# Performance work log

Hardware: AMD Instinct MI355X
Metric: run time of the kernel (lower is better)

The kernel has to match this reference:

```python
import jax, jax.numpy as jnp
import numpy as np


def _rotate_every_two(x):
    # interleaved pairs: (x0, x1) -> (-x1, x0)
    x1 = x[..., ::2]
    x2 = x[..., 1::2]
    return jnp.stack((-x2, x1), axis=-1).reshape(x.shape)


def setup_inputs() -> dict:
    key = jax.random.key(0)
    ks = jax.random.split(key, 6)
    B, S, D = 2, 2048, 1024
    w = lambda k, shape: jax.random.normal(k, shape, dtype=jnp.float32) * 0.02
    return {
        "x": jax.random.normal(ks[0], (B, S, D), dtype=jnp.float32),
        "Wq": w(ks[1], (D, D)), "bq": jnp.zeros((D,), jnp.float32),
        "Wk": w(ks[2], (D, D)), "bk": jnp.zeros((D,), jnp.float32),
        "Wv": w(ks[3], (D, 2 * D)), "bv": jnp.zeros((2 * D,), jnp.float32),
        "Wg": w(ks[4], (D, 2 * D)), "bg": jnp.zeros((2 * D,), jnp.float32),
        "Wo": w(ks[5], (2 * D, D)), "bo": jnp.zeros((D,), jnp.float32),
    }


def reference(x, Wq, bq, Wk, bk, Wv, bv, Wg, bg, Wo, bo):
    B, S, D = x.shape
    H = 16
    key_dim = D // H          # 64
    head_dim = 2 * D // H     # 128 (factor=2)
    scaling = key_dim ** -0.5

    # RetNetRelPos buffers (deterministic)
    angle = 1.0 / 10000.0 ** jnp.linspace(0.0, 1.0, key_dim // 2)
    angle = jnp.repeat(angle, 2).astype(jnp.float32)          # [key_dim]
    decay = jnp.log(1.0 - 2.0 ** (-5.0 - jnp.arange(H, dtype=jnp.float32)))  # [H]

    idx = jnp.arange(S, dtype=jnp.float32)
    sin = jnp.sin(idx[:, None] * angle[None, :])              # [S, key_dim]
    cos = jnp.cos(idx[:, None] * angle[None, :])

    # causal exponential decay mask, normalized by sqrt(rowsum)
    diff = idx[:, None] - idx[None, :]                        # [S, S]
    mask = jnp.where(diff >= 0, jnp.exp(decay[:, None, None] * diff), 0.0)  # [H,S,S]
    mask = mask / jnp.sqrt(mask.sum(-1, keepdims=True))

    q = (x @ Wq + bq).reshape(B, S, H, key_dim).transpose(0, 2, 1, 3)              # [B,H,S,kd]
    k = ((x @ Wk + bk) * scaling).reshape(B, S, H, key_dim).transpose(0, 2, 1, 3)
    v = x @ Wv + bv                                                                # [B,S,2D]
    g = x @ Wg + bg

    qr = q * cos + _rotate_every_two(q) * sin
    kr = k * cos + _rotate_every_two(k) * sin
    vr = v.reshape(B, S, H, head_dim).transpose(0, 2, 1, 3)                        # [B,H,S,hd]

    qk = jnp.einsum('bhsd,bhtd->bhst', qr, kr) * mask                              # [B,H,S,S]
    denom = jnp.clip(jnp.abs(jax.lax.stop_gradient(qk).sum(-1, keepdims=True)), 1.0, None)
    qk = qk / denom

    out = jnp.einsum('bhst,bhtd->bhsd', qk, vr).transpose(0, 2, 1, 3)              # [B,S,H,hd]

    # LayerNorm over head_dim, eps=1e-5, no affine (biased variance as in torch)
    mu = out.mean(-1, keepdims=True)
    var = ((out - mu) ** 2).mean(-1, keepdims=True)
    out = (out - mu) / jnp.sqrt(var + 1e-5)

    out = out.reshape(B, S, H * head_dim)                                          # [B,S,2D]
    out = jax.nn.silu(g) * out
    return out @ Wo + bo
```

## Files before the change

kernel.cpp:

```cpp
#include <hip/hip_runtime.h>
#include <hip/hip_bf16.h>

typedef __attribute__((ext_vector_type(8))) unsigned short ushort8;
typedef __attribute__((ext_vector_type(4))) float f32x4;
typedef __attribute__((ext_vector_type(8))) __bf16 bf16x8;
typedef unsigned int u32_g __attribute__((address_space(1)));
typedef unsigned int u32_l __attribute__((address_space(3)));

__device__ __forceinline__ float bf2f(unsigned short u) {
  union { unsigned u; float f; } v; v.u = ((unsigned)u) << 16; return v.f;
}
__device__ __forceinline__ unsigned short f2bf(float f) {
  union { float f; unsigned u; } v; v.f = f;
  unsigned r = v.u + 0x7FFFu + ((v.u >> 16) & 1u);
  return (unsigned short)(r >> 16);
}
__device__ __forceinline__ unsigned cvtpk_bf16(float lo, float hi) {
  unsigned r;
  asm("v_cvt_pk_bf16_f32 %0, %1, %2" : "=v"(r) : "v"(lo), "v"(hi));
  return r;
}
__device__ __forceinline__ f32x4 mfma16(bf16x8 a, bf16x8 b, f32x4 c) {
  return __builtin_amdgcn_mfma_f32_16x16x32_bf16(a, b, c, 0, 0, 0);
}
__device__ __forceinline__ void gload16(const void* g, void* l) {
  __builtin_amdgcn_global_load_lds((const u32_g*)g, (u32_l*)l, 16, 0, 0);
}

__global__ __launch_bounds__(256) void transpose_cast(
    const float* __restrict__ W, unsigned short* __restrict__ WT,
    int K, int N, int ldwt, int row_off)
{
  __shared__ unsigned short t[64 * 80];
  int n0 = blockIdx.x * 64, k0 = blockIdx.y * 64;
  int tid = threadIdx.x;
#pragma unroll
  for (int i = 0; i < 4; i++) {
    int c = tid + 256 * i;
    int r = c >> 4, q = c & 15;
    float4 v = *(const float4*)&W[(size_t)(k0 + r) * N + n0 + q * 4];
    t[(q * 4 + 0) * 80 + r] = f2bf(v.x);
    t[(q * 4 + 1) * 80 + r] = f2bf(v.y);
    t[(q * 4 + 2) * 80 + r] = f2bf(v.z);
    t[(q * 4 + 3) * 80 + r] = f2bf(v.w);
  }
  __syncthreads();
#pragma unroll
  for (int i = 0; i < 2; i++) {
    int c = tid + 256 * i;
    int n = c >> 3, p = c & 7;
    *(ushort8*)&WT[(size_t)(row_off + n0 + n) * ldwt + k0 + p * 8] =
        *(const ushort8*)&t[n * 80 + p * 8];
  }
}

__global__ void biascat_kernel(const float* __restrict__ bq, const float* __restrict__ bk,
                               const float* __restrict__ bv, const float* __restrict__ bg,
                               float* __restrict__ bcat)
{
  int i = blockIdx.x * 256 + threadIdx.x;
  float v;
  if (i < 1024) v = bq[i];
  else if (i < 2048) v = bk[i - 1024];
  else if (i < 4096) v = bv[i - 2048];
  else v = bg[i - 4096];
  bcat[i] = v;
}

__global__ void cast_x_kernel(const float* __restrict__ x, unsigned short* __restrict__ xb)
{
  size_t i = (size_t)(blockIdx.x * 256 + threadIdx.x) * 4;
  float4 v = *(const float4*)&x[i];
  unsigned r0 = (unsigned)f2bf(v.x) | ((unsigned)f2bf(v.y) << 16);
  unsigned r1 = (unsigned)f2bf(v.z) | ((unsigned)f2bf(v.w) << 16);
  uint2 o; o.x = r0; o.y = r1;
  *(uint2*)&xb[i] = o;
}

template<int OUT_BF16, int BN, int SM, int SN>
__global__ __launch_bounds__(256, 3) void gemm3_kernel(
    const unsigned short* __restrict__ A, const unsigned short* __restrict__ BT,
    const float* __restrict__ bias, void* __restrict__ Cout,
    int M, int N, int K)
{
  constexpr int BUFS = (128 + BN) * 32;
  constexpr int ACH  = 512;
  constexpr int LPS  = (128 + BN) / 64;
  constexpr int STB  = SM * SN;
  __shared__ __attribute__((aligned(16))) unsigned short lds[3 * BUFS];
  int tid = threadIdx.x, wave = tid >> 6, lane = tid & 63;
  int lr = lane & 15, lg = lane >> 4;
  int gx = gridDim.x;
  int lin = blockIdx.x + gx * blockIdx.y;
  int cpx = (gx * gridDim.y) >> 3;
  int xcd = lin & 7, s = lin >> 3;
  int spx = cpx / STB;
  int sup = xcd * spx + s / STB;
  int nSupN = gx / SN;
  int stm = sup / nSupN, stn = sup % nSupN;
  int idx = s % STB;
  int m0 = (stm * SM + idx / SN) * 128;
  int n0 = (stn * SN + idx % SN) * BN;
  int wr = (wave >> 1) * 64, wc = (wave & 1) * (BN / 2);
  constexpr int NR = BN / 32;

  const unsigned short* gsrc[LPS];
#pragma unroll
  for (int i = 0; i < LPS; i++) {
    int c = tid + i * 256;
    if (c < ACH) {
      int r = c >> 2, j = c & 3;
      gsrc[i] = A + (size_t)(m0 + r) * K + ((j ^ ((r >> 1) & 3)) << 3);
    } else {
      int c2 = c - ACH, r = c2 >> 2, j = c2 & 3;
      gsrc[i] = BT + (size_t)(n0 + r) * K + ((j ^ ((r >> 1) & 3)) << 3);
    }
  }

  auto stage = [&](int buf, int kt) {
    char* lb = (char*)(lds + buf * BUFS);
#pragma unroll
    for (int i = 0; i < LPS; i++)
      gload16(gsrc[i] + kt * 32, lb + (tid + i * 256) * 16);
  };

  f32x4 acc[4][NR] = {};
  int nk = K >> 5;
  stage(0, 0);
  stage(1, 1);
  int cb = 0;
  for (int it = 0; it < nk; it++) {
    if (it + 1 < nk) {
      if constexpr (LPS == 4) asm volatile("s_waitcnt vmcnt(4)" ::: "memory");
      else                    asm volatile("s_waitcnt vmcnt(3)" ::: "memory");
    } else {
      asm volatile("s_waitcnt vmcnt(0)" ::: "memory");
    }
    __builtin_amdgcn_sched_barrier(0);
    __builtin_amdgcn_s_barrier();
    __builtin_amdgcn_sched_barrier(0);
    if (it + 2 < nk) {
      int sb = cb + 2; if (sb >= 3) sb -= 3;
      stage(sb, it + 2);
    }
    const unsigned short* as = lds + cb * BUFS;
    const unsigned short* bs = as + 128 * 32;
    int csw = (lg ^ ((lr >> 1) & 3)) << 3;
    bf16x8 af[4], bfr[NR];
#pragma unroll
    for (int m = 0; m < 4; m++)
      af[m] = *(const bf16x8*)&as[(wr + m * 16 + lr) * 32 + csw];
#pragma unroll
    for (int n = 0; n < NR; n++)
      bfr[n] = *(const bf16x8*)&bs[(wc + n * 16 + lr) * 32 + csw];
    __builtin_amdgcn_s_setprio(1);
#pragma unroll
    for (int m = 0; m < 4; m++)
#pragma unroll
      for (int n = 0; n < NR; n++)
        acc[m][n] = mfma16(af[m], bfr[n], acc[m][n]);
    __builtin_amdgcn_s_setprio(0);
    cb++; if (cb == 3) cb = 0;
  }

#pragma unroll
  for (int m = 0; m < 4; m++) {
#pragma unroll
    for (int n = 0; n < NR; n++) {
      int col = n0 + wc + n * 16 + lr;
      float bv = bias ? bias[col] : 0.f;
#pragma unroll
      for (int r = 0; r < 4; r++) {
        int row = m0 + wr + m * 16 + lg * 4 + r;
        float v = acc[m][n][r] + bv;
        if (OUT_BF16)
          ((unsigned short*)Cout)[(size_t)row * N + col] = f2bf(v);
        else
          ((float*)Cout)[(size_t)row * N + col] = v;
      }
    }
  }
}

__global__ __launch_bounds__(256) void prep_qk_kernel(
    const unsigned short* __restrict__ Y,
    unsigned short* __restrict__ qr, unsigned short* __restrict__ kr)
{
  int t = blockIdx.x * 256 + threadIdx.x;
  int j = t & 31;
  int h = (t >> 5) & 15;
  int bs = t >> 9;
  int s = bs & 2047;
  int b = bs >> 11;
  float ang = __expf(-0.29710774f * (float)j);
  float th = (float)s * ang;
  float sn, cs;
  __sincosf(th, &sn, &cs);
  const unsigned short* yq = &Y[(size_t)bs * 6144 + h * 64 + 2 * j];
  unsigned qv = *(const unsigned*)yq;
  unsigned kv = *(const unsigned*)(yq + 1024);
  float q0 = bf2f((unsigned short)(qv & 0xffff));
  float q1 = bf2f((unsigned short)(qv >> 16));
  float k0 = bf2f((unsigned short)(kv & 0xffff)) * 0.125f;
  float k1 = bf2f((unsigned short)(kv >> 16)) * 0.125f;
  float qr0 = q0 * cs - q1 * sn, qr1 = q1 * cs + q0 * sn;
  float kr0 = k0 * cs - k1 * sn, kr1 = k1 * cs + k0 * sn;
  size_t o = ((size_t)(b * 16 + h) * 2048 + s) * 64 + 2 * j;
  *(unsigned*)&qr[o] = (unsigned)f2bf(qr0) | ((unsigned)f2bf(qr1) << 16);
  *(unsigned*)&kr[o] = (unsigned)f2bf(kr0) | ((unsigned)f2bf(kr1) << 16);
}

__global__ __launch_bounds__(256) void prep_v_kernel(
    const unsigned short* __restrict__ Y, unsigned short* __restrict__ vT)
{
  __shared__ unsigned short t[128 * 80];
  int s0 = blockIdx.x * 64;
  int bh = blockIdx.y;
  int b = bh >> 4, h = bh & 15;
  int tid = threadIdx.x;
#pragma unroll
  for (int i = 0; i < 4; i++) {
    int c = tid + 256 * i;
    int r = c >> 4, p = c & 15;
    ushort8 v = *(const ushort8*)&Y[(size_t)(b * 2048 + s0 + r) * 6144 + 2048 + h * 128 + p * 8];
#pragma unroll
    for (int e = 0; e < 8; e++) t[(p * 8 + e) * 80 + r] = v[e];
  }
  __syncthreads();
#pragma unroll
  for (int i = 0; i < 4; i++) {
    int c = tid + 256 * i;
    int d = c >> 3, p = c & 7;
    *(ushort8*)&vT[((size_t)bh * 128 + d) * 2048 + s0 + p * 8] = *(const ushort8*)&t[d * 80 + p * 8];
  }
}

#define LPAD 72
__global__ __launch_bounds__(256, 2) void retention_kernel(
    const unsigned short* __restrict__ qr, const unsigned short* __restrict__ kr,
    const unsigned short* __restrict__ vT, const unsigned short* __restrict__ Yg,
    unsigned short* __restrict__ Z)
{
  __shared__ __attribute__((aligned(16))) unsigned short lds[24576 + 4 * 16 * LPAD];
  unsigned short* const lk0 = lds;
  unsigned short* const lk1 = lds + 4096;
  unsigned short* const lv0 = lds + 8192;
  unsigned short* const lv1 = lds + 16384;
  unsigned short* const lp  = lds + 24576;

  int lin = blockIdx.x;
  int xcd = lin & 7, slot = lin >> 3;
  int bh = xcd + 8 * (slot >> 4);
  int bx = slot & 15;
  int b = bh >> 4, h = bh & 15;
  float decay = __logf(1.f - exp2f(-5.f - (float)h));
  int tid = threadIdx.x, wave = tid >> 6, lane = tid & 63;
  int lr = lane & 15, lg = lane >> 4;
  const unsigned short* qbase = &qr[(size_t)bh * 2048 * 64];
  const unsigned short* kbase = &kr[(size_t)bh * 2048 * 64];
  const unsigned short* vbase = &vT[(size_t)bh * 128 * 2048];
  unsigned short* lpw = &lp[wave * 16 * LPAD];
  int swz = (lr & 7) << 3;

  float cf[4][4];
#pragma unroll
  for (int nb = 0; nb < 4; nb++)
#pragma unroll
    for (int r = 0; r < 4; r++)
      cf[nb][r] = __expf(-decay * (float)(nb * 16 + lg * 4 + r));

  auto stage = [&](int bufi, int t0) {
    const char* kg = (const char*)(kbase + (size_t)t0 * 64);
    const char* vg = (const char*)vbase + (size_t)t0 * 2;
    char* lk = (char*)(bufi ? lk1 : lk0);
    char* lv = (char*)(bufi ? lv1 : lv0);
#pragma unroll
    for (int i = 0; i < 2; i++) {
      int c = tid + i * 256;
      int r = c >> 3, j = c & 7;
      gload16(kg + r * 128 + ((j ^ (r & 7)) << 4), lk + c * 16);
    }
#pragma unroll
    for (int i = 0; i < 4; i++) {
      int c = tid + i * 256;
      int d = c >> 3, j = c & 7;
      gload16(vg + (size_t)d * 4096 + ((j ^ (d & 7)) << 4), lv + c * 16);
    }
  };

  for (int pass = 0; pass < 2; pass++) {
    int stile = pass ? 31 - bx : bx;
    int s0 = stile * 64;
    int sq = s0 + wave * 16 + lr;
    bf16x8 qf0 = *(const bf16x8*)&qbase[(size_t)sq * 64 + lg * 8];
    bf16x8 qf1 = *(const bf16x8*)&qbase[(size_t)sq * 64 + 32 + lg * 8];
    f32x4 accv[8] = {};
    float rs = 0.f;
    int nt = stile + 1;

    stage(0, 0);
    __syncthreads();
    for (int it = 0; it < nt; it++) {
      int t0 = it * 64;
      if (it + 1 < nt) stage((it + 1) & 1, t0 + 64);
      const unsigned short* lk = (it & 1) ? lk1 : lk0;
      const unsigned short* lv = (it & 1) ? lv1 : lv0;
      bool bnd = (it == nt - 1);
      float rowf = __expf(decay * (float)(sq - t0));
#pragma unroll
      for (int nb = 0; nb < 4; nb++) {
        f32x4 sa = {};
        bf16x8 a0 = *(const bf16x8*)&lk[((nb * 16 + lr) * 64 + lg * 8) ^ swz];
        bf16x8 a1 = *(const bf16x8*)&lk[((nb * 16 + lr) * 64 + 32 + lg * 8) ^ swz];
        sa = mfma16(a0, qf0, sa);
        sa = mfma16(a1, qf1, sa);
        float pv[4];
#pragma unroll
        for (int r = 0; r < 4; r++) {
          float w = rowf * cf[nb][r];
          if (bnd) {
            int tt = t0 + nb * 16 + lg * 4 + r;
            w = (tt <= sq) ? w : 0.f;
          }
          pv[r] = sa[r] * w;
          rs += pv[r];
        }
        uint2 wv;
        wv.x = cvtpk_bf16(pv[0], pv[1]);
        wv.y = cvtpk_bf16(pv[2], pv[3]);
        *(uint2*)&lpw[lr * LPAD + nb * 16 + lg * 4] = wv;
      }
#pragma unroll
      for (int kk = 0; kk < 2; kk++) {
        bf16x8 pa = *(const bf16x8*)&lpw[lr * LPAD + kk * 32 + lg * 8];
#pragma unroll
        for (int nb = 0; nb < 8; nb++) {
          bf16x8 bv = *(const bf16x8*)&lv[((nb * 16 + lr) * 64 + kk * 32 + lg * 8) ^ swz];
          accv[nb] = mfma16(pa, bv, accv[nb]);
        }
      }
      __syncthreads();
    }

    rs += __shfl_xor(rs, 16);
    rs += __shfl_xor(rs, 32);
    int srb = s0 + wave * 16 + lg * 4;
    const unsigned short* gb2 = &Yg[((size_t)(b * 2048 + srb)) * 6144 + 4096 + h * 128];
    unsigned short* zb = &Z[((size_t)(b * 2048 + srb)) * 2048 + h * 128];
#pragma unroll
    for (int r = 0; r < 4; r++) {
      float rsq = __shfl(rs, lg * 4 + r);
      float sidx = (float)(srb + r);
      float geo = (1.f - __expf(decay * (sidx + 1.f))) * exp2f(5.f + (float)h);
      float invs = rsqrtf(geo);
      float den = fmaxf(fabsf(rsq * invs), 1.f);
      float scl = invs / den;
      float sm = 0.f, sq2 = 0.f;
#pragma unroll
      for (int nb = 0; nb < 8; nb++) {
        float v = accv[nb][r] * scl;
        sm += v; sq2 += v * v;
      }
      sm += __shfl_xor(sm, 1); sm += __shfl_xor(sm, 2);
      sm += __shfl_xor(sm, 4); sm += __shfl_xor(sm, 8);
      sq2 += __shfl_xor(sq2, 1); sq2 += __shfl_xor(sq2, 2);
      sq2 += __shfl_xor(sq2, 4); sq2 += __shfl_xor(sq2, 8);
      float mu = sm * (1.f / 128.f);
      float var = sq2 * (1.f / 128.f) - mu * mu;
      float istd = rsqrtf(var + 1e-5f);
#pragma unroll
      for (int nb = 0; nb < 8; nb++) {
        float v = accv[nb][r] * scl;
        float nrm = (v - mu) * istd;
        float g = bf2f(gb2[(size_t)r * 6144 + nb * 16 + lr]);
        float sg = g / (1.f + __expf(-g));
        zb[(size_t)r * 2048 + nb * 16 + lr] = f2bf(nrm * sg);
      }
    }
  }
}

extern "C" void kernel_launch(void* const* d_in, const int* in_sizes, int n_in,
                              void* d_out, int out_size, void* d_ws, size_t ws_size,
                              hipStream_t stream) {
  const float* x  = (const float*)d_in[0];
  const float* Wq = (const float*)d_in[1];
  const float* bq = (const float*)d_in[2];
  const float* Wk = (const float*)d_in[3];
  const float* bk = (const float*)d_in[4];
  const float* Wv = (const float*)d_in[5];
  const float* bv = (const float*)d_in[6];
  const float* Wg = (const float*)d_in[7];
  const float* bg = (const float*)d_in[8];
  const float* Wo = (const float*)d_in[9];
  const float* bo = (const float*)d_in[10];

  char* ws = (char*)d_ws;
  unsigned short* xbf   = (unsigned short*)(ws);
  unsigned short* wcatT = (unsigned short*)(ws + 8388608);
  unsigned short* woT   = (unsigned short*)(ws + 20971520);
  unsigned short* Y     = (unsigned short*)(ws + 25165824);
  unsigned short* qrb   = (unsigned short*)(ws + 75497472);
  unsigned short* krb   = (unsigned short*)(ws + 83886080);
  unsigned short* vT    = (unsigned short*)(ws + 92274688);
  float*          bcat  = (float*)(ws + 109051904);
  unsigned short* Z     = xbf;

  transpose_cast<<<dim3(16, 16), 256, 0, stream>>>(Wq, wcatT, 1024, 1024, 1024, 0);
  transpose_cast<<<dim3(16, 16), 256, 0, stream>>>(Wk, wcatT, 1024, 1024, 1024, 1024);
  transpose_cast<<<dim3(32, 16), 256, 0, stream>>>(Wv, wcatT, 1024, 2048, 1024, 2048);
  transpose_cast<<<dim3(32, 16), 256, 0, stream>>>(Wg, wcatT, 1024, 2048, 1024, 4096);
  transpose_cast<<<dim3(16, 32), 256, 0, stream>>>(Wo, woT, 2048, 1024, 2048, 0);
  biascat_kernel<<<24, 256, 0, stream>>>(bq, bk, bv, bg, bcat);
  cast_x_kernel<<<4096, 256, 0, stream>>>(x, xbf);

  gemm3_kernel<1, 128, 8, 6><<<dim3(48, 32), 256, 0, stream>>>(xbf, wcatT, bcat, Y, 4096, 6144, 1024);

  prep_qk_kernel<<<8192, 256, 0, stream>>>(Y, qrb, krb);
  prep_v_kernel<<<dim3(32, 32), 256, 0, stream>>>(Y, vT);

  retention_kernel<<<512, 256, 0, stream>>>(qrb, krb, vT, Y, Z);

  gemm3_kernel<0, 64, 4, 4><<<dim3(16, 32), 256, 0, stream>>>(Z, woT, bo, d_out, 4096, 1024, 2048);
}
```

Before: 197.1 us.

## Switch retention kernel to 32x32 MFMA with 128-row query tiles

Rewrites the retention kernel to use 32x32x16 bf16 MFMA instructions, with each wave owning 32 query rows and each block owning a 128-row query tile instead of two 64-row passes. Load balancing changes from pairing tiles within one head to pairing mirrored tiles across two heads. The P tile gets an XOR-swizzled LDS layout in place of padding. The aim is fewer LDS reads and MFMA issues per FLOP, since K/V tiles are reused across more query rows. The cost is more accumulator registers (4 f32x16) and a boundary mask that now covers two tiles.

```diff
diff --git a/kernel.cpp b/kernel.cpp
--- a/kernel.cpp
+++ b/kernel.cpp
@@ -3,6 +3,7 @@
 
 typedef __attribute__((ext_vector_type(8))) unsigned short ushort8;
 typedef __attribute__((ext_vector_type(4))) float f32x4;
+typedef __attribute__((ext_vector_type(16))) float f32x16;
 typedef __attribute__((ext_vector_type(8))) __bf16 bf16x8;
 typedef unsigned int u32_g __attribute__((address_space(1)));
 typedef unsigned int u32_l __attribute__((address_space(3)));
@@ -22,6 +23,9 @@
 }
 __device__ __forceinline__ f32x4 mfma16(bf16x8 a, bf16x8 b, f32x4 c) {
   return __builtin_amdgcn_mfma_f32_16x16x32_bf16(a, b, c, 0, 0, 0);
+}
+__device__ __forceinline__ f32x16 mfma32(bf16x8 a, bf16x8 b, f32x16 c) {
+  return __builtin_amdgcn_mfma_f32_32x32x16_bf16(a, b, c, 0, 0, 0);
 }
 __device__ __forceinline__ void gload16(const void* g, void* l) {
   __builtin_amdgcn_global_load_lds((const u32_g*)g, (u32_l*)l, 16, 0, 0);
@@ -235,13 +239,12 @@
   }
 }
 
-#define LPAD 72
 __global__ __launch_bounds__(256, 2) void retention_kernel(
     const unsigned short* __restrict__ qr, const unsigned short* __restrict__ kr,
     const unsigned short* __restrict__ vT, const unsigned short* __restrict__ Yg,
     unsigned short* __restrict__ Z)
 {
-  __shared__ __attribute__((aligned(16))) unsigned short lds[24576 + 4 * 16 * LPAD];
+  __shared__ __attribute__((aligned(16))) unsigned short lds[24576 + 4 * 32 * 64];
   unsigned short* const lk0 = lds;
   unsigned short* const lk1 = lds + 4096;
   unsigned short* const lv0 = lds + 8192;
@@ -249,25 +252,33 @@
   unsigned short* const lp  = lds + 24576;
 
   int lin = blockIdx.x;
-  int xcd = lin & 7, slot = lin >> 3;
-  int bh = xcd + 8 * (slot >> 4);
-  int bx = slot & 15;
+  int xcd = lin & 7, s = lin >> 3;
+  int par = s & 1, j = (s >> 1) & 15, bg = s >> 5;
+  int f  = par ? 15 - j : j;
+  int bh = xcd + 8 * (2 * bg + par);
   int b = bh >> 4, h = bh & 15;
   float decay = __logf(1.f - exp2f(-5.f - (float)h));
   int tid = threadIdx.x, wave = tid >> 6, lane = tid & 63;
-  int lr = lane & 15, lg = lane >> 4;
+  int lq = lane & 31, hi = lane >> 5;
   const unsigned short* qbase = &qr[(size_t)bh * 2048 * 64];
   const unsigned short* kbase = &kr[(size_t)bh * 2048 * 64];
   const unsigned short* vbase = &vT[(size_t)bh * 128 * 2048];
-  unsigned short* lpw = &lp[wave * 16 * LPAD];
-  int swz = (lr & 7) << 3;
-
-  float cf[4][4];
-#pragma unroll
-  for (int nb = 0; nb < 4; nb++)
-#pragma unroll
-    for (int r = 0; r < 4; r++)
-      cf[nb][r] = __expf(-decay * (float)(nb * 16 + lg * 4 + r));
+  unsigned short* lpw = &lp[wave * 32 * 64];
+  int kswz = lq & 7;
+  int pswz = (lq & 7) << 1;
+
+  int q0 = f * 128;
+  int sq = q0 + wave * 32 + lq;
+  bf16x8 qf[4];
+#pragma unroll
+  for (int ks = 0; ks < 4; ks++)
+    qf[ks] = *(const bf16x8*)&qbase[(size_t)sq * 64 + hi * 8 + ks * 16];
+
+  float cfA[16];
+#pragma unroll
+  for (int r = 0; r < 16; r++)
+    cfA[r] = __expf(-decay * (float)((r & 3) + 8 * (r >> 2) + 4 * hi));
+  float w32 = __expf(-decay * 32.f);
 
   auto stage = [&](int bufi, int t0) {
     const char* kg = (const char*)(kbase + (size_t)t0 * 64);
@@ -277,105 +288,114 @@
 #pragma unroll
     for (int i = 0; i < 2; i++) {
       int c = tid + i * 256;
-      int r = c >> 3, j = c & 7;
-      gload16(kg + r * 128 + ((j ^ (r & 7)) << 4), lk + c * 16);
+      int r = c >> 3, jj = c & 7;
+      gload16(kg + r * 128 + ((jj ^ (r & 7)) << 4), lk + c * 16);
     }
 #pragma unroll
     for (int i = 0; i < 4; i++) {
       int c = tid + i * 256;
-      int d = c >> 3, j = c & 7;
-      gload16(vg + (size_t)d * 4096 + ((j ^ (d & 7)) << 4), lv + c * 16);
+      int d = c >> 3, jj = c & 7;
+      gload16(vg + (size_t)d * 4096 + ((jj ^ (d & 7)) << 4), lv + c * 16);
     }
   };
 
-  for (int pass = 0; pass < 2; pass++) {
-    int stile = pass ? 31 - bx : bx;
-    int s0 = stile * 64;
-    int sq = s0 + wave * 16 + lr;
-    bf16x8 qf0 = *(const bf16x8*)&qbase[(size_t)sq * 64 + lg * 8];
-    bf16x8 qf1 = *(const bf16x8*)&qbase[(size_t)sq * 64 + 32 + lg * 8];
-    f32x4 accv[8] = {};
-    float rs = 0.f;
-    int nt = stile + 1;
-
-    stage(0, 0);
+  f32x16 accv[4] = {};
+  float rs = 0.f;
+  int nt = 2 * f + 2;
+
+  stage(0, 0);
+  __syncthreads();
+  for (int it = 0; it < nt; it++) {
+    int t0 = it * 64;
+    if (it + 1 < nt) stage((it + 1) & 1, t0 + 64);
+    const unsigned short* lk = (it & 1) ? lk1 : lk0;
+    const unsigned short* lv = (it & 1) ? lv1 : lv0;
+    bool bnd = (it >= nt - 2);
+    float rowf = __expf(decay * (float)(sq - t0));
+    f32x16 st0 = {}, st1 = {};
+#pragma unroll
+    for (int ks = 0; ks < 4; ks++) {
+      bf16x8 a0 = *(const bf16x8*)&lk[lq * 64 + (((hi + 2 * ks) ^ kswz) << 3)];
+      bf16x8 a1 = *(const bf16x8*)&lk[(32 + lq) * 64 + (((hi + 2 * ks) ^ kswz) << 3)];
+      st0 = mfma32(a0, qf[ks], st0);
+      st1 = mfma32(a1, qf[ks], st1);
+    }
+#pragma unroll
+    for (int tb = 0; tb < 2; tb++) {
+      float rf = tb ? rowf * w32 : rowf;
+#pragma unroll
+      for (int g = 0; g < 4; g++) {
+        float p0, p1, p2, p3;
+        {
+          float w0 = rf * cfA[g * 4 + 0];
+          float w1 = rf * cfA[g * 4 + 1];
+          float w2 = rf * cfA[g * 4 + 2];
+          float w3 = rf * cfA[g * 4 + 3];
+          if (bnd) {
+            int tb0 = t0 + 32 * tb + 8 * g + 4 * hi;
+            w0 = (tb0 + 0 <= sq) ? w0 : 0.f;
+            w1 = (tb0 + 1 <= sq) ? w1 : 0.f;
+            w2 = (tb0 + 2 <= sq) ? w2 : 0.f;
+            w3 = (tb0 + 3 <= sq) ? w3 : 0.f;
+          }
+          const f32x16& stv = tb ? st1 : st0;
+          p0 = stv[g * 4 + 0] * w0;
+          p1 = stv[g * 4 + 1] * w1;
+          p2 = stv[g * 4 + 2] * w2;
+          p3 = stv[g * 4 + 3] * w3;
+        }
+        rs += p0 + p1 + p2 + p3;
+        uint2 wv;
+        wv.x = cvtpk_bf16(p0, p1);
+        wv.y = cvtpk_bf16(p2, p3);
+        int c4 = (2 * g + hi + 8 * tb) ^ pswz;
+        *(uint2*)&lpw[lq * 64 + (c4 << 2)] = wv;
+      }
+    }
+#pragma unroll
+    for (int ts = 0; ts < 4; ts++) {
+      bf16x8 pa = *(const bf16x8*)&lpw[lq * 64 + ((((2 * hi + 4 * ts)) ^ pswz) << 2)];
+#pragma unroll
+      for (int nb = 0; nb < 4; nb++) {
+        bf16x8 vf = *(const bf16x8*)&lv[(nb * 32 + lq) * 64 + (((hi + 2 * ts) ^ kswz) << 3)];
+        accv[nb] = mfma32(pa, vf, accv[nb]);
+      }
+    }
     __syncthreads();
-    for (int it = 0; it < nt; it++) {
-      int t0 = it * 64;
-      if (it + 1 < nt) stage((it + 1) & 1, t0 + 64);
-      const unsigned short* lk = (it & 1) ? lk1 : lk0;
-      const unsigned short* lv = (it & 1) ? lv1 : lv0;
-      bool bnd = (it == nt - 1);
-      float rowf = __expf(decay * (float)(sq - t0));
-#pragma unroll
-      for (int nb = 0; nb < 4; nb++) {
-        f32x4 sa = {};
-        bf16x8 a0 = *(const bf16x8*)&lk[((nb * 16 + lr) * 64 + lg * 8) ^ swz];
-        bf16x8 a1 = *(const bf16x8*)&lk[((nb * 16 + lr) * 64 + 32 + lg * 8) ^ swz];
-        sa = mfma16(a0, qf0, sa);
-        sa = mfma16(a1, qf1, sa);
-        float pv[4];
-#pragma unroll
-        for (int r = 0; r < 4; r++) {
-          float w = rowf * cf[nb][r];
-          if (bnd) {
-            int tt = t0 + nb * 16 + lg * 4 + r;
-            w = (tt <= sq) ? w : 0.f;
-          }
-          pv[r] = sa[r] * w;
-          rs += pv[r];
-        }
-        uint2 wv;
-        wv.x = cvtpk_bf16(pv[0], pv[1]);
-        wv.y = cvtpk_bf16(pv[2], pv[3]);
-        *(uint2*)&lpw[lr * LPAD + nb * 16 + lg * 4] = wv;
-      }
-#pragma unroll
-      for (int kk = 0; kk < 2; kk++) {
-        bf16x8 pa = *(const bf16x8*)&lpw[lr * LPAD + kk * 32 + lg * 8];
-#pragma unroll
-        for (int nb = 0; nb < 8; nb++) {
-          bf16x8 bv = *(const bf16x8*)&lv[((nb * 16 + lr) * 64 + kk * 32 + lg * 8) ^ swz];
-          accv[nb] = mfma16(pa, bv, accv[nb]);
-        }
-      }
-      __syncthreads();
-    }
-
-    rs += __shfl_xor(rs, 16);
-    rs += __shfl_xor(rs, 32);
-    int srb = s0 + wave * 16 + lg * 4;
-    const unsigned short* gb2 = &Yg[((size_t)(b * 2048 + srb)) * 6144 + 4096 + h * 128];
-    unsigned short* zb = &Z[((size_t)(b * 2048 + srb)) * 2048 + h * 128];
-#pragma unroll
-    for (int r = 0; r < 4; r++) {
-      float rsq = __shfl(rs, lg * 4 + r);
-      float sidx = (float)(srb + r);
-      float geo = (1.f - __expf(decay * (sidx + 1.f))) * exp2f(5.f + (float)h);
-      float invs = rsqrtf(geo);
-      float den = fmaxf(fabsf(rsq * invs), 1.f);
-      float scl = invs / den;
-      float sm = 0.f, sq2 = 0.f;
-#pragma unroll
-      for (int nb = 0; nb < 8; nb++) {
-        float v = accv[nb][r] * scl;
-        sm += v; sq2 += v * v;
-      }
-      sm += __shfl_xor(sm, 1); sm += __shfl_xor(sm, 2);
-      sm += __shfl_xor(sm, 4); sm += __shfl_xor(sm, 8);
-      sq2 += __shfl_xor(sq2, 1); sq2 += __shfl_xor(sq2, 2);
-      sq2 += __shfl_xor(sq2, 4); sq2 += __shfl_xor(sq2, 8);
-      float mu = sm * (1.f / 128.f);
-      float var = sq2 * (1.f / 128.f) - mu * mu;
-      float istd = rsqrtf(var + 1e-5f);
-#pragma unroll
-      for (int nb = 0; nb < 8; nb++) {
-        float v = accv[nb][r] * scl;
-        float nrm = (v - mu) * istd;
-        float g = bf2f(gb2[(size_t)r * 6144 + nb * 16 + lr]);
-        float sg = g / (1.f + __expf(-g));
-        zb[(size_t)r * 2048 + nb * 16 + lr] = f2bf(nrm * sg);
-      }
+  }
+
+  rs += __shfl_xor(rs, 32);
+#pragma unroll
+  for (int r = 0; r < 16; r++) {
+    int rowloc = (r & 3) + 8 * (r >> 2) + 4 * hi;
+    int sqr = q0 + wave * 32 + rowloc;
+    float rsr = __shfl(rs, rowloc);
+    float geo = (1.f - __expf(decay * ((float)sqr + 1.f))) * exp2f(5.f + (float)h);
+    float invs = rsqrtf(geo);
+    float den = fmaxf(fabsf(rsr * invs), 1.f);
+    float scl = invs / den;
+    float sm = 0.f, s2 = 0.f;
+#pragma unroll
+    for (int nb = 0; nb < 4; nb++) {
+      float v = accv[nb][r] * scl;
+      sm += v; s2 += v * v;
+    }
+    sm += __shfl_xor(sm, 1); sm += __shfl_xor(sm, 2);
+    sm += __shfl_xor(sm, 4); sm += __shfl_xor(sm, 8); sm += __shfl_xor(sm, 16);
+    s2 += __shfl_xor(s2, 1); s2 += __shfl_xor(s2, 2);
+    s2 += __shfl_xor(s2, 4); s2 += __shfl_xor(s2, 8); s2 += __shfl_xor(s2, 16);
+    float mu = sm * (1.f / 128.f);
+    float var = s2 * (1.f / 128.f) - mu * mu;
+    float istd = rsqrtf(var + 1e-5f);
+    const unsigned short* grow = &Yg[((size_t)(b * 2048 + sqr)) * 6144 + 4096 + h * 128 + lq];
+    unsigned short* zrow = &Z[((size_t)(b * 2048 + sqr)) * 2048 + h * 128 + lq];
+#pragma unroll
+    for (int nb = 0; nb < 4; nb++) {
+      float v = accv[nb][r] * scl;
+      float nrm = (v - mu) * istd;
+      float g = bf2f(grow[nb * 32]);
+      float sg = g / (1.f + __expf(-g));
+      zrow[nb * 32] = f2bf(nrm * sg);
     }
   }
 }
```

Measured after the change: 207.2 us. +5.1%, slower.
